# Performance work log

Measured on AMD Instinct MI355X. Metric: run time of the kernel, lower is better.

Reference implementation:

```python
import jax, jax.numpy as jnp
import numpy as np

NUM_CLASSES = 100            # num_classes (no-object class index == NUM_CLASSES)
MIN_PAIR_W = 0.1             # min_point_pair_weight
EPS = 1e-8


def setup_inputs() -> dict:
    key = jax.random.key(0)
    ks = jax.random.split(key, 8)
    B, Q, C1 = 16, 200, NUM_CLASSES + 1
    M = 800                  # matched GT instances across the batch
    NPTS = 200000            # sampled pixel points (per-point query-logit vectors)
    P = 500000               # point pairs for the clustering loss
    pred_logits = jax.random.normal(ks[0], (B, Q, C1), dtype=jnp.float32)
    targets = jax.random.randint(ks[1], (M,), 0, NUM_CLASSES)
    idx_b = jax.random.randint(ks[2], (M,), 0, B)
    idx_q = jax.random.randint(ks[3], (M,), 0, Q)
    src_clusters = jax.random.normal(ks[4], (NPTS, Q), dtype=jnp.float32)
    pairs = jax.random.randint(ks[5], (P, 2), 0, NPTS)
    pair_pos = jax.random.bernoulli(ks[6], 0.5, (P,))
    pair_weights = jax.random.uniform(ks[7], (P,), dtype=jnp.float32)
    # empty_weight buffer: ones with eos_coef on the no-object class
    empty_weight = jnp.ones((C1,), dtype=jnp.float32).at[-1].set(0.1)
    return {"pred_logits": pred_logits, "targets": targets, "idx_b": idx_b,
            "idx_q": idx_q, "src_clusters": src_clusters, "pairs": pairs,
            "pair_pos": pair_pos, "pair_weights": pair_weights,
            "empty_weight": empty_weight}


def _loss_labels(pred_logits, targets, idx_b, idx_q, empty_weight):
    B, Q, _ = pred_logits.shape
    # target_classes = full(no-object); target_classes[indices] = targets
    target_classes = jnp.full((B, Q), NUM_CLASSES, dtype=jnp.int32)
    target_classes = target_classes.at[idx_b, idx_q].set(targets.astype(jnp.int32))
    logp = jax.nn.log_softmax(pred_logits.astype(jnp.float32), axis=-1)  # [B,Q,C+1]
    nll = -jnp.take_along_axis(logp, target_classes[..., None], axis=-1)[..., 0]
    w = empty_weight[target_classes]
    # torch weighted cross_entropy: sum(w*nll)/sum(w)
    return jnp.sum(w * nll) / jnp.sum(w)


def _loss_clusters(src_clusters, pairs, pair_pos, pair_weights):
    a = src_clusters[pairs[:, 0]]            # [P,Q] gather
    b = src_clusters[pairs[:, 1]]            # [P,Q] gather
    cos = jnp.sum(a * b, axis=-1) / (
        jnp.linalg.norm(a, axis=-1) * jnp.linalg.norm(b, axis=-1) + EPS)
    w = jnp.maximum(pair_weights, MIN_PAIR_W)
    per_pair = jnp.where(pair_pos, 1.0 - cos, jnp.maximum(cos, 0.0))
    return jnp.sum(w * per_pair) / jnp.sum(w)


def reference(pred_logits, targets, idx_b, idx_q, src_clusters, pairs,
              pair_pos, pair_weights, empty_weight):
    loss_ce = _loss_labels(pred_logits, targets, idx_b, idx_q, empty_weight)
    loss_cluster = _loss_clusters(src_clusters, pairs, pair_pos, pair_weights)
    return loss_ce + loss_cluster
```

## Files before the change

kernel.cpp:

```cpp
#include <hip/hip_runtime.h>
#include <math.h>

#define NUM_CLASSES_ 100
#define C1_ 101
#define BQ_ 3200
#define QDIM_ 200
#define ROW_DW 64

static __device__ __forceinline__ int dot8i8(uint2 a, uint2 b) {
#if __has_builtin(__builtin_amdgcn_sdot4)
    int s = __builtin_amdgcn_sdot4(a.x, b.x, 0, false);
    return __builtin_amdgcn_sdot4(a.y, b.y, s, false);
#else
    int s = 0;
    #pragma unroll
    for (int k = 0; k < 4; ++k) {
        int av = (int)(a.x << (24 - 8 * k)) >> 24;
        int bv = (int)(b.x << (24 - 8 * k)) >> 24;
        int aw = (int)(a.y << (24 - 8 * k)) >> 24;
        int bw = (int)(b.y << (24 - 8 * k)) >> 24;
        s += av * bv + aw * bw;
    }
    return s;
#endif
}

__global__ void init_kernel(float* acc, int* tc) {
    int i = blockIdx.x * blockDim.x + threadIdx.x;
    if (i < 4) acc[i] = 0.0f;
    if (i < BQ_) tc[i] = -1;
}

__global__ void scatter_kernel(const int* __restrict__ targets,
                               const int* __restrict__ idx_b,
                               const int* __restrict__ idx_q,
                               int* tc, int M) {
    int m = blockIdx.x * blockDim.x + threadIdx.x;
    if (m < M) {
        int slot = idx_b[m] * QDIM_ + idx_q[m];
        atomicMax(&tc[slot], (m << 8) | targets[m]);
    }
}

__global__ __launch_bounds__(256) void ce_kernel(const float* __restrict__ logits,
                                                 const int* __restrict__ tc,
                                                 const float* __restrict__ empty_w,
                                                 float* acc) {
    int lane = threadIdx.x & 63;
    int gw = (blockIdx.x * blockDim.x + threadIdx.x) >> 6;
    int nw = (gridDim.x * blockDim.x) >> 6;
    float lnum = 0.0f, lden = 0.0f;
    for (int row = gw; row < BQ_; row += nw) {
        const float* x = logits + (size_t)row * C1_;
        float x0 = x[lane];
        bool has2 = (lane < C1_ - 64);
        float x1 = has2 ? x[lane + 64] : -INFINITY;
        float m = fmaxf(x0, x1);
        #pragma unroll
        for (int off = 32; off; off >>= 1) m = fmaxf(m, __shfl_xor(m, off));
        float s = expf(x0 - m) + (has2 ? expf(x1 - m) : 0.0f);
        #pragma unroll
        for (int off = 32; off; off >>= 1) s += __shfl_xor(s, off);
        int packed = tc[row];
        int cls = (packed >= 0) ? (packed & 255) : NUM_CLASSES_;
        float xt = x[cls];
        float nll = -(xt - m - logf(s));
        float w = empty_w[cls];
        lnum += w * nll;
        lden += w;
    }
    if (lane == 0) { atomicAdd(&acc[0], lnum); atomicAdd(&acc[1], lden); }
}

__global__ __launch_bounds__(256) void quantize_kernel(const float* __restrict__ src,
                                                       unsigned int* __restrict__ qtab,
                                                       float* __restrict__ invq, int npts) {
    int lane = threadIdx.x & 63;
    int gw = (blockIdx.x * blockDim.x + threadIdx.x) >> 6;
    int nw = (gridDim.x * blockDim.x) >> 6;
    for (int r = gw; r < npts; r += nw) {
        float4 a = make_float4(0.f, 0.f, 0.f, 0.f);
        float s = 0.0f;
        if (lane < QDIM_ / 4) {
            a = reinterpret_cast<const float4*>(src + (size_t)r * QDIM_)[lane];
            s = a.x * a.x + a.y * a.y + a.z * a.z + a.w * a.w;
        }
        #pragma unroll
        for (int off = 32; off; off >>= 1) s += __shfl_xor(s, off);
        float inv = rsqrtf(s);
        inv = inv * (1.5f - 0.5f * s * inv * inv);
        float sc = inv * 127.0f;
        int q0 = (int)rintf(a.x * sc);
        int q1 = (int)rintf(a.y * sc);
        int q2 = (int)rintf(a.z * sc);
        int q3 = (int)rintf(a.w * sc);
        unsigned int packed = (unsigned)(q0 & 255) | ((unsigned)(q1 & 255) << 8)
                            | ((unsigned)(q2 & 255) << 16) | ((unsigned)(q3 & 255) << 24);
        int sq = q0 * q0 + q1 * q1 + q2 * q2 + q3 * q3;
        #pragma unroll
        for (int off = 32; off; off >>= 1) sq += __shfl_xor(sq, off);
        qtab[(size_t)r * ROW_DW + lane] = (lane < QDIM_ / 4) ? packed : 0u;
        if (lane == 0) {
            float fs = (float)sq;
            float iv = rsqrtf(fs);
            iv = iv * (1.5f - 0.5f * fs * iv * iv);
            invq[r] = iv;
        }
    }
}

__global__ __launch_bounds__(256) void pair_i8_kernel(const uint2* __restrict__ qtab,
                                                      const int2* __restrict__ pairs2,
                                                      const int* __restrict__ pos,
                                                      const float* __restrict__ pw,
                                                      const float* __restrict__ invq,
                                                      float* acc, int P) {
    int lane = threadIdx.x & 63;
    int gw = (blockIdx.x * blockDim.x + threadIdx.x) >> 6;
    int nw = (gridDim.x * blockDim.x) >> 6;
    int chunk = (P + nw - 1) / nw;
    int pbeg = gw * chunk;
    int pend = min(P, pbeg + chunk);
    float num = 0.0f, den = 0.0f;

    int2 prA = {0, 0}, prB = {0, 0}, prC = {0, 0}, prD = {0, 0};
    uint2 vA = {0, 0}, vB = {0, 0}, vC = {0, 0}, vD = {0, 0};

    auto refill = [&](int idx, int2& pr, uint2& v) {
        if (idx < pend) {
            int i = __builtin_amdgcn_readfirstlane(idx);
            pr = pairs2[i];
            int row = (lane < 32) ? pr.x : pr.y;
            v = qtab[(size_t)row * 32 + (lane & 31)];
        }
    };
    auto process = [&](int2 pr, uint2 v, int idx) {
        uint2 w;
        w.x = (unsigned)__shfl_xor((int)v.x, 32);
        w.y = (unsigned)__shfl_xor((int)v.y, 32);
        int d = dot8i8(v, w);
        #pragma unroll
        for (int off = 16; off; off >>= 1) d += __shfl_xor(d, off);
        int i = __builtin_amdgcn_readfirstlane(idx);
        float cosv = (float)d * invq[__builtin_amdgcn_readfirstlane(pr.x)]
                              * invq[__builtin_amdgcn_readfirstlane(pr.y)];
        float per = pos[i] ? (1.0f - cosv) : fmaxf(cosv, 0.0f);
        float wgt = fmaxf(pw[i], 0.1f);
        num += wgt * per;
        den += wgt;
    };

    refill(pbeg,     prA, vA);
    refill(pbeg + 1, prB, vB);
    refill(pbeg + 2, prC, vC);
    refill(pbeg + 3, prD, vD);
    for (int p = pbeg; p < pend; p += 4) {
        process(prA, vA, p);
        refill(p + 4, prA, vA);
        if (p + 1 < pend) process(prB, vB, p + 1);
        refill(p + 5, prB, vB);
        if (p + 2 < pend) process(prC, vC, p + 2);
        refill(p + 6, prC, vC);
        if (p + 3 < pend) process(prD, vD, p + 3);
        refill(p + 7, prD, vD);
    }

    __shared__ float snum[4], sden[4];
    int wib = threadIdx.x >> 6;
    if (lane == 0) { snum[wib] = num; sden[wib] = den; }
    __syncthreads();
    if (threadIdx.x == 0) {
        atomicAdd(&acc[2], snum[0] + snum[1] + snum[2] + snum[3]);
        atomicAdd(&acc[3], sden[0] + sden[1] + sden[2] + sden[3]);
    }
}

__global__ __launch_bounds__(256) void pair_fp32_kernel(const float* __restrict__ src,
                                                        const int* __restrict__ pairs,
                                                        const int* __restrict__ pos,
                                                        const float* __restrict__ pw,
                                                        float* acc, int P) {
    int lane = threadIdx.x & 63;
    int gw = (blockIdx.x * blockDim.x + threadIdx.x) >> 6;
    int nw = (gridDim.x * blockDim.x) >> 6;
    float num = 0.0f, den = 0.0f;
    for (int p = gw; p < P; p += nw) {
        int2 pr = reinterpret_cast<const int2*>(pairs)[p];
        float dot = 0.0f, saa = 0.0f, sbb = 0.0f;
        if (lane < QDIM_ / 4) {
            float4 a = reinterpret_cast<const float4*>(src + (size_t)pr.x * QDIM_)[lane];
            float4 b = reinterpret_cast<const float4*>(src + (size_t)pr.y * QDIM_)[lane];
            dot = a.x * b.x + a.y * b.y + a.z * b.z + a.w * b.w;
            saa = a.x * a.x + a.y * a.y + a.z * a.z + a.w * a.w;
            sbb = b.x * b.x + b.y * b.y + b.z * b.z + b.w * b.w;
        }
        #pragma unroll
        for (int off = 32; off; off >>= 1) {
            dot += __shfl_xor(dot, off);
            saa += __shfl_xor(saa, off);
            sbb += __shfl_xor(sbb, off);
        }
        float cosv = dot / (sqrtf(saa) * sqrtf(sbb) + 1e-8f);
        float per = pos[p] ? (1.0f - cosv) : fmaxf(cosv, 0.0f);
        float w = fmaxf(pw[p], 0.1f);
        num += w * per;
        den += w;
    }
    __shared__ float snum[4], sden[4];
    int wib = threadIdx.x >> 6;
    if (lane == 0) { snum[wib] = num; sden[wib] = den; }
    __syncthreads();
    if (threadIdx.x == 0) {
        atomicAdd(&acc[2], snum[0] + snum[1] + snum[2] + snum[3]);
        atomicAdd(&acc[3], sden[0] + sden[1] + sden[2] + sden[3]);
    }
}

__global__ void final_kernel(const float* __restrict__ acc, float* out) {
    if (threadIdx.x == 0 && blockIdx.x == 0)
        out[0] = acc[0] / acc[1] + acc[2] / acc[3];
}

extern "C" void kernel_launch(void* const* d_in, const int* in_sizes, int n_in,
                              void* d_out, int out_size, void* d_ws, size_t ws_size,
                              hipStream_t stream) {
    const float* pred_logits = (const float*)d_in[0];
    const int*   targets     = (const int*)d_in[1];
    const int*   idx_b       = (const int*)d_in[2];
    const int*   idx_q       = (const int*)d_in[3];
    const float* src         = (const float*)d_in[4];
    const int*   pairs       = (const int*)d_in[5];
    const int*   pair_pos    = (const int*)d_in[6];
    const float* pair_w      = (const float*)d_in[7];
    const float* empty_w     = (const float*)d_in[8];
    float* out = (float*)d_out;

    int M = in_sizes[1];
    int P = in_sizes[7];
    int npts = in_sizes[4] / QDIM_;

    float* acc = (float*)d_ws;
    int*   tc  = (int*)((char*)d_ws + 16);
    unsigned int* qtab = (unsigned int*)((char*)d_ws + 16384);
    float* invq = (float*)((char*)d_ws + 16384 + (size_t)npts * 256);

    init_kernel<<<(BQ_ + 255) / 256, 256, 0, stream>>>(acc, tc);
    scatter_kernel<<<(M + 255) / 256, 256, 0, stream>>>(targets, idx_b, idx_q, tc, M);
    ce_kernel<<<100, 256, 0, stream>>>(pred_logits, tc, empty_w, acc);

    bool i8 = ws_size >= (size_t)16384 + (size_t)npts * 256 + (size_t)npts * 4;
    if (i8) {
        quantize_kernel<<<2048, 256, 0, stream>>>(src, qtab, invq, npts);
        pair_i8_kernel<<<2048, 256, 0, stream>>>((const uint2*)qtab, (const int2*)pairs,
                                                 pair_pos, pair_w, invq, acc, P);
    } else {
        pair_fp32_kernel<<<2048, 256, 0, stream>>>(src, pairs, pair_pos, pair_w, acc, P);
    }
    final_kernel<<<1, 64, 0, stream>>>(acc, out);
}
```

Baseline: 405.7 us.

## Compute int8 pair dot products with MFMA 16x16x64 over 16-pair chunks

Measured after the change: 356.3 us. -12.2%, faster.

```diff
diff --git a/kernel.cpp b/kernel.cpp
--- a/kernel.cpp
+++ b/kernel.cpp
@@ -6,6 +6,8 @@
 #define BQ_ 3200
 #define QDIM_ 200
 #define ROW_DW 64
+
+typedef __attribute__((ext_vector_type(4))) int i32x4;
 
 static __device__ __forceinline__ int dot8i8(uint2 a, uint2 b) {
 #if __has_builtin(__builtin_amdgcn_sdot4)
@@ -109,62 +111,59 @@
     }
 }
 
-__global__ __launch_bounds__(256) void pair_i8_kernel(const uint2* __restrict__ qtab,
-                                                      const int2* __restrict__ pairs2,
-                                                      const int* __restrict__ pos,
-                                                      const float* __restrict__ pw,
-                                                      const float* __restrict__ invq,
-                                                      float* acc, int P) {
-    int lane = threadIdx.x & 63;
-    int gw = (blockIdx.x * blockDim.x + threadIdx.x) >> 6;
-    int nw = (gridDim.x * blockDim.x) >> 6;
-    int chunk = (P + nw - 1) / nw;
-    int pbeg = gw * chunk;
-    int pend = min(P, pbeg + chunk);
+__global__ __launch_bounds__(256) void pair_mfma_kernel(const uint4* __restrict__ qtab4,
+                                                        const int2* __restrict__ pairs2,
+                                                        const int* __restrict__ pos,
+                                                        const float* __restrict__ pw,
+                                                        const float* __restrict__ invq,
+                                                        float* acc, int P) {
+    int lane = threadIdx.x & 63;
+    int i15 = lane & 15;
+    int grp = lane >> 4;
+    int gw = (blockIdx.x * blockDim.x + threadIdx.x) >> 6;
+    int nw = (gridDim.x * blockDim.x) >> 6;
+    int nchunks = (P + 15) / 16;
+
+    int myreg = i15 - (grp << 2);
+    bool owns = (myreg >= 0) && (myreg < 4);
+
     float num = 0.0f, den = 0.0f;
 
-    int2 prA = {0, 0}, prB = {0, 0}, prC = {0, 0}, prD = {0, 0};
-    uint2 vA = {0, 0}, vB = {0, 0}, vC = {0, 0}, vD = {0, 0};
-
-    auto refill = [&](int idx, int2& pr, uint2& v) {
-        if (idx < pend) {
-            int i = __builtin_amdgcn_readfirstlane(idx);
-            pr = pairs2[i];
-            int row = (lane < 32) ? pr.x : pr.y;
-            v = qtab[(size_t)row * 32 + (lane & 31)];
-        }
-    };
-    auto process = [&](int2 pr, uint2 v, int idx) {
-        uint2 w;
-        w.x = (unsigned)__shfl_xor((int)v.x, 32);
-        w.y = (unsigned)__shfl_xor((int)v.y, 32);
-        int d = dot8i8(v, w);
-        #pragma unroll
-        for (int off = 16; off; off >>= 1) d += __shfl_xor(d, off);
-        int i = __builtin_amdgcn_readfirstlane(idx);
-        float cosv = (float)d * invq[__builtin_amdgcn_readfirstlane(pr.x)]
-                              * invq[__builtin_amdgcn_readfirstlane(pr.y)];
-        float per = pos[i] ? (1.0f - cosv) : fmaxf(cosv, 0.0f);
-        float wgt = fmaxf(pw[i], 0.1f);
-        num += wgt * per;
-        den += wgt;
-    };
-
-    refill(pbeg,     prA, vA);
-    refill(pbeg + 1, prB, vB);
-    refill(pbeg + 2, prC, vC);
-    refill(pbeg + 3, prD, vD);
-    for (int p = pbeg; p < pend; p += 4) {
-        process(prA, vA, p);
-        refill(p + 4, prA, vA);
-        if (p + 1 < pend) process(prB, vB, p + 1);
-        refill(p + 5, prB, vB);
-        if (p + 2 < pend) process(prC, vC, p + 2);
-        refill(p + 6, prC, vC);
-        if (p + 3 < pend) process(prD, vD, p + 3);
-        refill(p + 7, prD, vD);
-    }
-
+    for (int c = gw; c < nchunks; c += nw) {
+        int base = c * 16;
+        int p = base + i15;
+        int pc = min(p, P - 1);
+        int2 pr = pairs2[pc];
+        const uint4* arow = qtab4 + (size_t)pr.x * 16;
+        const uint4* brow = qtab4 + (size_t)pr.y * 16;
+
+        uint4 a0 = arow[grp];        uint4 b0 = brow[grp];
+        uint4 a1 = arow[4 + grp];    uint4 b1 = brow[4 + grp];
+        uint4 a2 = arow[8 + grp];    uint4 b2 = brow[8 + grp];
+        uint4 a3 = arow[12 + grp];   uint4 b3 = brow[12 + grp];
+
+        i32x4 macc = {0, 0, 0, 0};
+        macc = __builtin_amdgcn_mfma_i32_16x16x64_i8(*(i32x4*)&a0, *(i32x4*)&b0, macc, 0, 0, 0);
+        macc = __builtin_amdgcn_mfma_i32_16x16x64_i8(*(i32x4*)&a1, *(i32x4*)&b1, macc, 0, 0, 0);
+        macc = __builtin_amdgcn_mfma_i32_16x16x64_i8(*(i32x4*)&a2, *(i32x4*)&b2, macc, 0, 0, 0);
+        macc = __builtin_amdgcn_mfma_i32_16x16x64_i8(*(i32x4*)&a3, *(i32x4*)&b3, macc, 0, 0, 0);
+
+        if (owns && p < P) {
+            int d = (myreg == 0) ? macc[0] : (myreg == 1) ? macc[1]
+                  : (myreg == 2) ? macc[2] : macc[3];
+            float cosv = (float)d * invq[pr.x] * invq[pr.y];
+            float per = pos[p] ? (1.0f - cosv) : fmaxf(cosv, 0.0f);
+            float w = fmaxf(pw[p], 0.1f);
+            num += w * per;
+            den += w;
+        }
+    }
+
+    #pragma unroll
+    for (int off = 32; off; off >>= 1) {
+        num += __shfl_xor(num, off);
+        den += __shfl_xor(den, off);
+    }
     __shared__ float snum[4], sden[4];
     int wib = threadIdx.x >> 6;
     if (lane == 0) { snum[wib] = num; sden[wib] = den; }
@@ -246,13 +245,13 @@
 
     init_kernel<<<(BQ_ + 255) / 256, 256, 0, stream>>>(acc, tc);
     scatter_kernel<<<(M + 255) / 256, 256, 0, stream>>>(targets, idx_b, idx_q, tc, M);
-    ce_kernel<<<100, 256, 0, stream>>>(pred_logits, tc, empty_w, acc);
+    ce_kernel<<<200, 256, 0, stream>>>(pred_logits, tc, empty_w, acc);
 
     bool i8 = ws_size >= (size_t)16384 + (size_t)npts * 256 + (size_t)npts * 4;
     if (i8) {
         quantize_kernel<<<2048, 256, 0, stream>>>(src, qtab, invq, npts);
-        pair_i8_kernel<<<2048, 256, 0, stream>>>((const uint2*)qtab, (const int2*)pairs,
-                                                 pair_pos, pair_w, invq, acc, P);
+        pair_mfma_kernel<<<2048, 256, 0, stream>>>((const uint4*)qtab, (const int2*)pairs,
+                                                   pair_pos, pair_w, invq, acc, P);
     } else {
         pair_fp32_kernel<<<2048, 256, 0, stream>>>(src, pairs, pair_pos, pair_w, acc, P);
     }
```
